# Kernel tuning notes

Hardware: AMD Instinct MI355X
Metric: run time of the kernel (lower is better)

Reference implementation:

```python
import jax, jax.numpy as jnp
import numpy as np

B, H, W = 2, 1024, 1024
NNZ = 100000          # active pixels
C = 16                # max electron count bins (dense dim of sparse logits)
CIN, CH = 128, 128    # in_pixel_features, beta_distn_hidden_dim
THR = 0.95            # count_cdf_threshold
QMAX = NNZ * (C - 1)  # static upper bound on ragged query count


def setup_inputs() -> dict:
    key = jax.random.key(0)
    ks = jax.random.split(key, 4)
    rng = np.random.default_rng(0)
    per = NNZ // B
    idx_list = []
    for b in range(B):
        flat = np.sort(rng.choice(H * W, per, replace=False))  # unique active sites
        idx_list.append(np.stack([np.full(per, b), flat // W, flat % W]))
    occ_indices = jnp.asarray(np.concatenate(idx_list, 1), jnp.int32)  # [3, NNZ]
    occ_values = jax.random.normal(ks[0], (NNZ, C), jnp.float32) * 2.0
    pixel_values = jax.random.normal(ks[1], (NNZ, CIN), jnp.float32)
    w1 = jax.random.normal(ks[2], (3, 3, CIN, CH), jnp.float32) / np.sqrt(9 * CIN)
    b1 = jnp.zeros((CH,), jnp.float32)
    w2 = jax.random.normal(ks[3], (CH, 4), jnp.float32) / np.sqrt(CH)
    b2 = jnp.zeros((4,), jnp.float32)
    return dict(occ_values=occ_values, occ_indices=occ_indices,
                pixel_values=pixel_values, w1=w1, b1=b1, w2=w2, b2=b2)


def reference(occ_values, occ_indices, pixel_values, w1, b1, w2, b2):
    # --- cdf_threshold_min_predicted_electrons ---
    probs = jax.nn.softmax(occ_values, -1)                      # sparse softmax over dense count dim
    cdf = jnp.cumsum(probs, -1)
    over = cdf > THR
    temp = jnp.arange(C, 0, -1) * over
    counts = jnp.argmax(temp, 1)                                # [NNZ] min count over cdf threshold

    # --- repeat_interleave(indices, counts) -> padded ragged queries ---
    cum = jnp.cumsum(counts)
    total = cum[-1]
    q = jnp.arange(QMAX)
    valid = q < total
    src = jnp.minimum(jnp.searchsorted(cum, q, side='right'), NNZ - 1)  # [QMAX]
    query_indices = occ_indices[:, src].T                       # [QMAX, 3] (b, i, j)

    # --- dense hash grid: (b,i,j) -> active-site row ---
    b_, i_, j_ = occ_indices
    flat = (b_ * H + i_) * W + j_
    grid = jnp.full((B * H * W,), -1, jnp.int32).at[flat].set(
        jnp.arange(NNZ, dtype=jnp.int32))

    # --- SubMConv2d(CIN->CH, k=3): output at active sites only ---
    acc = jnp.zeros((NNZ, CH), pixel_values.dtype) + b1
    for di in (-1, 0, 1):
        for dj in (-1, 0, 1):
            ni, nj = i_ + di, j_ + dj
            inb = (ni >= 0) & (ni < H) & (nj >= 0) & (nj < W)
            nflat = (b_ * H + jnp.clip(ni, 0, H - 1)) * W + jnp.clip(nj, 0, W - 1)
            nidx = jnp.where(inb, grid[nflat], -1)
            m = nidx >= 0
            feat = jnp.where(m[:, None], pixel_values[jnp.maximum(nidx, 0)], 0.0)
            acc = acc + feat @ w1[di + 1, dj + 1]
    h = jax.nn.relu(acc)
    logp = h @ w2 + b2                                          # [NNZ, 4] SubMConv2d(CH->4, k=1)

    # --- gather_from_sparse_tensor at query pixels ---
    qflat = (query_indices[:, 0] * H + query_indices[:, 1]) * W + query_indices[:, 2]
    row = jnp.maximum(grid[qflat], 0)
    params = jnp.exp(logp[row])                                 # [QMAX, 4]
    xa, xb, ya, yb = jnp.split(params, 4, -1)

    # --- Beta rsample (reparameterized gamma-based sampler) ---
    k1, k2 = jax.random.split(jax.random.key(42))
    x = jax.random.beta(k1, xa, xb)
    y = jax.random.beta(k2, ya, yb)
    off = jnp.concatenate([x, y], -1) * valid[:, None]          # [QMAX, 2]
    query_indices = jnp.where(valid[:, None], query_indices, 0)
    return query_indices, off
```

## Files before the change

kernel.cpp:

```cpp
#include <hip/hip_runtime.h>
#include <cstdint>

#define NNZ   100000
#define CBINS 16
#define HD    1024
#define WD    1024
#define CIN   128
#define CH    128
#define QMAX  (NNZ * (CBINS - 1))

struct Key { uint32_t a, b; };

__device__ __forceinline__ uint32_t rotl32(uint32_t v, int r) {
  return (v << r) | (v >> (32 - r));
}

__device__ __forceinline__ void tf_block(uint32_t k0, uint32_t k1,
                                         uint32_t x0, uint32_t x1,
                                         uint32_t& o0, uint32_t& o1) {
  uint32_t ks2 = k0 ^ k1 ^ 0x1BD11BDAu;
  x0 += k0; x1 += k1;
#define TF_RND(r) { x0 += x1; x1 = rotl32(x1, r); x1 ^= x0; }
  TF_RND(13) TF_RND(15) TF_RND(26) TF_RND(6)
  x0 += k1;  x1 += ks2 + 1u;
  TF_RND(17) TF_RND(29) TF_RND(16) TF_RND(24)
  x0 += ks2; x1 += k0 + 2u;
  TF_RND(13) TF_RND(15) TF_RND(26) TF_RND(6)
  x0 += k0;  x1 += k1 + 3u;
  TF_RND(17) TF_RND(29) TF_RND(16) TF_RND(24)
  x0 += k1;  x1 += ks2 + 4u;
  TF_RND(13) TF_RND(15) TF_RND(26) TF_RND(6)
  x0 += ks2; x1 += k0 + 5u;
#undef TF_RND
  o0 = x0; o1 = x1;
}

__device__ __forceinline__ Key tf_key(Key k, uint32_t chi, uint32_t clo) {
  Key r; tf_block(k.a, k.b, chi, clo, r.a, r.b); return r;
}

__device__ __forceinline__ uint32_t random_bits32(Key k) {
  uint32_t a, b; tf_block(k.a, k.b, 0u, 0u, a, b); return a ^ b;
}

__device__ __forceinline__ float bits_to_u01(uint32_t bits) {
  uint32_t fb = (bits >> 9) | 0x3F800000u;
  return __uint_as_float(fb) - 1.0f;
}

__device__ float erfinv32(float x) {
#pragma clang fp contract(off)
  float w = -log1pf(-(x * x));
  float p;
  if (w < 5.0f) {
    w = w - 2.5f;
    p = 2.81022636e-08f;
    p = 3.43273939e-07f  + p * w;
    p = -3.5233877e-06f  + p * w;
    p = -4.39150654e-06f + p * w;
    p = 0.00021858087f   + p * w;
    p = -0.00125372503f  + p * w;
    p = -0.00417768164f  + p * w;
    p = 0.246640727f     + p * w;
    p = 1.50140941f      + p * w;
  } else {
    w = sqrtf(w) - 3.0f;
    p = -0.000200214257f;
    p = 0.000100950558f  + p * w;
    p = 0.00134934322f   + p * w;
    p = -0.00367342844f  + p * w;
    p = 0.00573950773f   + p * w;
    p = -0.0076224613f   + p * w;
    p = 0.00943887047f   + p * w;
    p = 1.00167406f      + p * w;
    p = 2.83297682f      + p * w;
  }
  return p * x;
}

__device__ __forceinline__ float uniform01(Key k) {
  return bits_to_u01(random_bits32(k));
}

__device__ __forceinline__ float normal_f32(Key k) {
#pragma clang fp contract(off)
  const float LO = -0x1.fffffep-1f;
  float f = bits_to_u01(random_bits32(k));
  float u = f * 2.0f + LO;
  u = fmaxf(LO, u);
  return 1.4142135623730951f * erfinv32(u);
}

__device__ float loggamma_one(Key key, float alpha_orig) {
#pragma clang fp contract(off)
  bool boost = (alpha_orig >= 1.0f);
  float alpha = boost ? alpha_orig : (alpha_orig + 1.0f);
  const float OT = 0.3333333333333333f;
  float d = alpha - OT;
  float c = OT / sqrtf(d);

  Key knext = tf_key(key, 0u, 0u);
  Key ksub  = tf_key(key, 0u, 1u);
  float u_boost = uniform01(ksub);

  float X = 0.0f, V = 1.0f, U = 2.0f;
  while (true) {
    bool c1 = U >= (1.0f - 0.0331f * (X * X));
    bool c2 = logf(U) >= (X * 0.5f + d * ((1.0f - V) + logf(V)));
    if (!(c1 && c2)) break;
    Key kcur = knext;
    knext    = tf_key(kcur, 0u, 0u);
    Key xk   = tf_key(kcur, 0u, 1u);
    Key Uk   = tf_key(kcur, 0u, 2u);
    float x = 0.0f, v = -1.0f;
    while (v <= 0.0f) {
      Key nxk = tf_key(xk, 0u, 0u);
      Key sk  = tf_key(xk, 0u, 1u);
      xk = nxk;
      x = normal_f32(sk);
      v = 1.0f + x * c;
    }
    X = x * x;
    V = (v * v) * v;
    U = uniform01(Uk);
  }
  float log_samples = logf(d) + logf(V);
  float log_boost = 0.0f;
  if (!boost && u_boost != 0.0f)
    log_boost = logf(u_boost) * (1.0f / alpha_orig);
  return log_samples + log_boost;
}

__device__ float beta_sample(Key ka, Key kb, uint32_t q, float a, float b) {
#pragma clang fp contract(off)
  Key ga = tf_key(ka, 0u, q);
  Key gb = tf_key(kb, 0u, q);
  float la = loggamma_one(ga, a);
  float lb = loggamma_one(gb, b);
  float lm = fmaxf(la, lb);
  float ea = expf(la - lm);
  float eb = expf(lb - lm);
  return ea / (ea + eb);
}


__device__ __forceinline__ void ascan16(const float* a, float* out) {
  float r[8], r2[4], r3[2];
#pragma unroll
  for (int i = 0; i < 8; ++i) r[i] = a[2 * i] + a[2 * i + 1];
#pragma unroll
  for (int i = 0; i < 4; ++i) r2[i] = r[2 * i] + r[2 * i + 1];
  r3[0] = r2[0] + r2[1];
  r3[1] = r2[2] + r2[3];
  float r4 = r3[0] + r3[1];
  float s3[2] = {r3[0], r4};
  float s2[4] = {r2[0], s3[0], s3[0] + r2[2], s3[1]};
  float sr[8] = {r[0],          s2[0],
                 s2[0] + r[2],  s2[1],
                 s2[1] + r[4],  s2[2],
                 s2[2] + r[6],  s2[3]};
  out[0] = a[0];
#pragma unroll
  for (int i = 0; i < 8; ++i) out[2 * i + 1] = sr[i];
#pragma unroll
  for (int i = 0; i < 7; ++i) out[2 * i + 2] = sr[i] + a[2 * i + 2];
}

__global__ __launch_bounds__(256)
void counts_kernel(const float* __restrict__ occ_values,
                   const int* __restrict__ occ_idx,
                   int* __restrict__ counts,
                   int* __restrict__ flatall) {
  int i = blockIdx.x * 256 + threadIdx.x;
  if (i >= NNZ) return;
  const float4* vp = (const float4*)(occ_values + (size_t)i * CBINS);
  float4 q0 = vp[0], q1 = vp[1], q2 = vp[2], q3 = vp[3];
  float v[16] = {q0.x,q0.y,q0.z,q0.w, q1.x,q1.y,q1.z,q1.w,
                 q2.x,q2.y,q2.z,q2.w, q3.x,q3.y,q3.z,q3.w};
  float m = v[0];
#pragma unroll
  for (int k = 1; k < 16; ++k) m = fmaxf(m, v[k]);
  float e[16];
#pragma unroll
  for (int k = 0; k < 16; ++k) e[k] = expf(v[k] - m);
  float s = 0.0f;
#pragma unroll
  for (int k = 0; k < 16; ++k) s += e[k];
  float p[16], cdf[16];
#pragma unroll
  for (int k = 0; k < 16; ++k) p[k] = e[k] / s;
  ascan16(p, cdf);
  int cnt = 0; bool found = false;
#pragma unroll
  for (int k = 0; k < 16; ++k) {
    if (!found && cdf[k] > 0.95f) { found = true; cnt = k; }
  }
  counts[i] = found ? cnt : 0;
  int b_ = occ_idx[i], i_ = occ_idx[NNZ + i], j_ = occ_idx[2 * NNZ + i];
  flatall[i] = (b_ * HD + i_) * WD + j_;
}

#define SCAN_B 1024
__global__ __launch_bounds__(SCAN_B)
void scan_block_kernel(const int* __restrict__ counts, int* __restrict__ cum,
                       int* __restrict__ bsums) {
  __shared__ int sh[SCAN_B];
  int t = threadIdx.x;
  int i = blockIdx.x * SCAN_B + t;
  sh[t] = (i < NNZ) ? counts[i] : 0;
  __syncthreads();
  for (int off = 1; off < SCAN_B; off <<= 1) {
    int add = (t >= off) ? sh[t - off] : 0;
    __syncthreads();
    sh[t] += add;
    __syncthreads();
  }
  if (i < NNZ) cum[i] = sh[t];
  if (t == SCAN_B - 1) bsums[blockIdx.x] = sh[t];
}

__global__ void scan_sums_kernel(int* bsums, int nblocks) {
  __shared__ int sh[128];
  int t = threadIdx.x;
  sh[t] = (t < nblocks) ? bsums[t] : 0;
  __syncthreads();
  for (int off = 1; off < 128; off <<= 1) {
    int add = (t >= off) ? sh[t - off] : 0;
    __syncthreads();
    sh[t] += add;
    __syncthreads();
  }
  if (t < nblocks) bsums[t] = sh[t];
}

__global__ __launch_bounds__(SCAN_B)
void scan_add_kernel(int* cum, const int* __restrict__ bsums) {
  int b = blockIdx.x;
  if (b == 0) return;
  int i = b * SCAN_B + threadIdx.x;
  if (i < NNZ) cum[i] += bsums[b - 1];
}

__device__ __forceinline__ int find_site(const int* __restrict__ flatall, int tval) {
  int lo = 0, hi = NNZ;
  while (lo < hi) {
    int mid = (lo + hi) >> 1;
    if (flatall[mid] < tval) lo = mid + 1; else hi = mid;
  }
  return (lo < NNZ && flatall[lo] == tval) ? lo : -1;
}

__global__ __launch_bounds__(256)
void neighbors_kernel(const int* __restrict__ occ_idx,
                      const int* __restrict__ flatall,
                      int* __restrict__ rlist) {
  int s = blockIdx.x * 256 + threadIdx.x;
  if (s >= NNZ) return;
  int b_ = occ_idx[s], i_ = occ_idx[NNZ + s], j_ = occ_idx[2 * NNZ + s];
  int m = 0;
#pragma unroll
  for (int di = -1; di <= 1; ++di) {
#pragma unroll
    for (int dj = -1; dj <= 1; ++dj) {
      if (di == 0 && dj == 0) continue;
      int ni = i_ + di, nj = j_ + dj, r = -1;
      if ((unsigned)ni < HD && (unsigned)nj < WD)
        r = find_site(flatall, (b_ * HD + ni) * WD + nj);
      rlist[(size_t)s * 8 + m] = r;
      ++m;
    }
  }
}

__global__ __launch_bounds__(256)
void scatter_src_kernel(const int* __restrict__ counts,
                        const int* __restrict__ cum,
                        int* __restrict__ srcmap) {
  int s = blockIdx.x * 256 + threadIdx.x;
  if (s >= NNZ) return;
  int e = cum[s], c = counts[s];
  for (int q = e - c; q < e; ++q) srcmap[q] = s;
}

#define TSITES 64
#define HP     132
__global__ __launch_bounds__(256, 4)
void conv_fused_kernel(const float* __restrict__ pv,
                       const float* __restrict__ w1,
                       const float* __restrict__ b1,
                       const float* __restrict__ w2,
                       const float* __restrict__ b2,
                       const int* __restrict__ rlist,
                       float* __restrict__ logp) {
  __shared__ float smem[TSITES * HP];
  __shared__ int rl[TSITES * 8];
  float* Wsh = smem;
  float* h0  = smem;

  int base = blockIdx.x * TSITES;
  int t = threadIdx.x;

#pragma unroll
  for (int rep = 0; rep < 2; ++rep) {
    int e = t + rep * 256;
    int sc = base + (e >> 3);
    if (sc > NNZ - 1) sc = NNZ - 1;
    rl[e] = rlist[(size_t)sc * 8 + (e & 7)];
  }

  int ts = t >> 5, to = t & 31;
  float acc[8][4];
  {
    float4 bv = *(const float4*)(b1 + to * 4);
#pragma unroll
    for (int s8 = 0; s8 < 8; ++s8) {
      acc[s8][0] = bv.x; acc[s8][1] = bv.y; acc[s8][2] = bv.z; acc[s8][3] = bv.w;
    }
  }

  const float* prow[8];
#pragma unroll
  for (int s8 = 0; s8 < 8; ++s8) {
    int site = base + s8 * 8 + ts;
    if (site > NNZ - 1) site = NNZ - 1;
    prow[s8] = pv + (size_t)site * CIN;
  }

  const float* wc = w1 + 4 * CIN * CH;
  for (int k0 = 0; k0 < CIN; k0 += 32) {
    __syncthreads();
    {
      const float4* srcw = (const float4*)(wc + (size_t)k0 * CH);
      float4* dstw = (float4*)Wsh;
#pragma unroll
      for (int rep = 0; rep < 4; ++rep) dstw[t + rep * 256] = srcw[t + rep * 256];
    }
    __syncthreads();
#pragma unroll
    for (int kk = 0; kk < 32; kk += 4) {
      float4 wq0 = ((const float4*)(Wsh + (kk + 0) * CH))[to];
      float4 wq1 = ((const float4*)(Wsh + (kk + 1) * CH))[to];
      float4 wq2 = ((const float4*)(Wsh + (kk + 2) * CH))[to];
      float4 wq3 = ((const float4*)(Wsh + (kk + 3) * CH))[to];
#pragma unroll
      for (int s8 = 0; s8 < 8; ++s8) {
        float4 a4 = *(const float4*)(prow[s8] + k0 + kk);
        acc[s8][0] += a4.x * wq0.x; acc[s8][1] += a4.x * wq0.y;
        acc[s8][2] += a4.x * wq0.z; acc[s8][3] += a4.x * wq0.w;
        acc[s8][0] += a4.y * wq1.x; acc[s8][1] += a4.y * wq1.y;
        acc[s8][2] += a4.y * wq1.z; acc[s8][3] += a4.y * wq1.w;
        acc[s8][0] += a4.z * wq2.x; acc[s8][1] += a4.z * wq2.y;
        acc[s8][2] += a4.z * wq2.z; acc[s8][3] += a4.z * wq2.w;
        acc[s8][0] += a4.w * wq3.x; acc[s8][1] += a4.w * wq3.y;
        acc[s8][2] += a4.w * wq3.z; acc[s8][3] += a4.w * wq3.w;
      }
    }
  }

  __syncthreads();
#pragma unroll
  for (int s8 = 0; s8 < 8; ++s8) {
    *(float4*)(h0 + (s8 * 8 + ts) * HP + 4 * to) =
        make_float4(acc[s8][0], acc[s8][1], acc[s8][2], acc[s8][3]);
  }
  __syncthreads();

  int w = t >> 6, l = t & 63;
  for (int si = 0; si < 16; ++si) {
    int s = w * 16 + si;
    int site = base + s;
    if (site >= NNZ) break;
    float2 hv = *(const float2*)(h0 + s * HP + 2 * l);
    float ha = hv.x, hb = hv.y;
#pragma unroll
    for (int m = 0; m < 8; ++m) {
      int r = rl[s * 8 + m];
      if (r < 0) continue;
      int tap = (m < 4) ? m : m + 1;
      const float* wt = w1 + (size_t)tap * CIN * CH + 2 * l;
      const float* pr = pv + (size_t)r * CIN;
#pragma unroll 8
      for (int k = 0; k < CIN; k += 4) {
        float4 pq = *(const float4*)(pr + k);
        float2 wv0 = *(const float2*)(wt + (k + 0) * CH);
        float2 wv1 = *(const float2*)(wt + (k + 1) * CH);
        float2 wv2 = *(const float2*)(wt + (k + 2) * CH);
        float2 wv3 = *(const float2*)(wt + (k + 3) * CH);
        ha += pq.x * wv0.x; hb += pq.x * wv0.y;
        ha += pq.y * wv1.x; hb += pq.y * wv1.y;
        ha += pq.z * wv2.x; hb += pq.z * wv2.y;
        ha += pq.w * wv3.x; hb += pq.w * wv3.y;
      }
    }
    *(float2*)(h0 + s * HP + 2 * l) = make_float2(ha, hb);
  }
  __syncthreads();

  {
    int s = t & 63, j = t >> 6;
    int site = base + s;
    if (site < NNZ) {
      const float* hr = h0 + s * HP;
      float sum = 0.0f;
      for (int o = 0; o < CH; o += 2) {
        float2 hv = *(const float2*)(hr + o);
        sum += fmaxf(hv.x, 0.f) * w2[(o + 0) * 4 + j];
        sum += fmaxf(hv.y, 0.f) * w2[(o + 1) * 4 + j];
      }
      logp[(size_t)site * 4 + j] = sum + b2[j];
    }
  }
}

__global__ __launch_bounds__(256)
void query_kernel(const int* __restrict__ occ_idx,
                  const int* __restrict__ cum,
                  const int* __restrict__ srcmap,
                  const float* __restrict__ logp,
                  float* __restrict__ out_idx,
                  float* __restrict__ out_off) {
  int q = blockIdx.x * 256 + threadIdx.x;
  if (q >= QMAX) return;
  int total = cum[NNZ - 1];
  if (q >= total) {
    out_idx[(size_t)q * 3 + 0] = 0.0f;
    out_idx[(size_t)q * 3 + 1] = 0.0f;
    out_idx[(size_t)q * 3 + 2] = 0.0f;
    out_off[(size_t)q * 2 + 0] = 0.0f;
    out_off[(size_t)q * 2 + 1] = 0.0f;
    return;
  }
  int src = srcmap[q];
  out_idx[(size_t)q * 3 + 0] = (float)occ_idx[src];
  out_idx[(size_t)q * 3 + 1] = (float)occ_idx[NNZ + src];
  out_idx[(size_t)q * 3 + 2] = (float)occ_idx[2 * NNZ + src];

  float4 lp = *(const float4*)(logp + (size_t)src * 4);
  float p0 = expf(lp.x), p1 = expf(lp.y), p2 = expf(lp.z), p3 = expf(lp.w);

  Key root{0u, 42u};
  Key k1  = tf_key(root, 0u, 0u);
  Key k2  = tf_key(root, 0u, 1u);
  Key kxa = tf_key(k1, 0u, 0u);
  Key kxb = tf_key(k1, 0u, 1u);
  Key kya = tf_key(k2, 0u, 0u);
  Key kyb = tf_key(k2, 0u, 1u);

  float x = beta_sample(kxa, kxb, (uint32_t)q, p0, p1);
  float y = beta_sample(kya, kyb, (uint32_t)q, p2, p3);
  out_off[(size_t)q * 2 + 0] = x;
  out_off[(size_t)q * 2 + 1] = y;
}

extern "C" void kernel_launch(void* const* d_in, const int* in_sizes, int n_in,
                              void* d_out, int out_size, void* d_ws, size_t ws_size,
                              hipStream_t stream) {
  const float* occ_values = (const float*)d_in[0];
  const int*   occ_idx    = (const int*)d_in[1];
  const float* pv         = (const float*)d_in[2];
  const float* w1         = (const float*)d_in[3];
  const float* b1         = (const float*)d_in[4];
  const float* w2         = (const float*)d_in[5];
  const float* b2         = (const float*)d_in[6];

  char* ws = (char*)d_ws;
  auto alignup = [](size_t x) { return (x + 255) & ~(size_t)255; };
  size_t o = 0;
  int* counts  = (int*)(ws + o); o += alignup((size_t)NNZ * 4);
  int* cum     = (int*)(ws + o); o += alignup((size_t)NNZ * 4);
  int* flatall = (int*)(ws + o); o += alignup((size_t)NNZ * 4);
  int* bsums   = (int*)(ws + o); o += alignup(128 * 4);
  float* logp  = (float*)(ws + o); o += alignup((size_t)NNZ * 4 * sizeof(float));
  int* rlist   = (int*)(ws + o); o += alignup((size_t)NNZ * 8 * 4);
  int* srcmap  = (int*)(ws + o); o += alignup((size_t)QMAX * 4);

  float* out_idx = (float*)d_out;
  float* out_off = out_idx + (size_t)QMAX * 3;

  counts_kernel<<<(NNZ + 255) / 256, 256, 0, stream>>>(occ_values, occ_idx,
                                                       counts, flatall);
  int nsb = (NNZ + SCAN_B - 1) / SCAN_B;
  scan_block_kernel<<<nsb, SCAN_B, 0, stream>>>(counts, cum, bsums);
  scan_sums_kernel<<<1, 128, 0, stream>>>(bsums, nsb);
  scan_add_kernel<<<nsb, SCAN_B, 0, stream>>>(cum, bsums);
  neighbors_kernel<<<(NNZ + 255) / 256, 256, 0, stream>>>(occ_idx, flatall, rlist);
  scatter_src_kernel<<<(NNZ + 255) / 256, 256, 0, stream>>>(counts, cum, srcmap);
  conv_fused_kernel<<<(NNZ + TSITES - 1) / TSITES, 256, 0, stream>>>(
      pv, w1, b1, w2, b2, rlist, logp);
  query_kernel<<<(QMAX + 255) / 256, 256, 0, stream>>>(occ_idx, cum, srcmap,
                                                       logp, out_idx, out_off);
}
```

Measured before the change: 715.2 us.

## Compact active neighbor sites and software-pipeline neighbor-tap loads in conv kernel

Builds a per-block list of sites that have at least one non-center active neighbor, then lets the four waves stride over only those sites instead of a fixed 16 sites each. This balances work across waves and skips empty sites. The inner CIN loop is also rewritten to prefetch the next 8 input and weight values while computing the current ones, which adds register pressure. The order of sites in the list now depends on atomics, but each site's result does not depend on that order.

```diff
diff --git a/kernel.cpp b/kernel.cpp
--- a/kernel.cpp
+++ b/kernel.cpp
@@ -294,12 +294,15 @@
                        float* __restrict__ logp) {
   __shared__ float smem[TSITES * HP];
   __shared__ int rl[TSITES * 8];
+  __shared__ int asl[TSITES];
+  __shared__ int aslN;
   float* Wsh = smem;
   float* h0  = smem;
 
   int base = blockIdx.x * TSITES;
   int t = threadIdx.x;
 
+  if (t == 0) aslN = 0;
 #pragma unroll
   for (int rep = 0; rep < 2; ++rep) {
     int e = t + rep * 256;
@@ -365,11 +368,21 @@
   }
   __syncthreads();
 
+  if (t < TSITES) {
+    bool any = false;
+#pragma unroll
+    for (int m = 0; m < 8; ++m) any |= (rl[t * 8 + m] >= 0);
+    if (any) {
+      int slot = atomicAdd(&aslN, 1);
+      asl[slot] = t;
+    }
+  }
+  __syncthreads();
+
   int w = t >> 6, l = t & 63;
-  for (int si = 0; si < 16; ++si) {
-    int s = w * 16 + si;
-    int site = base + s;
-    if (site >= NNZ) break;
+  int nact = aslN;
+  for (int e = w; e < nact; e += 4) {
+    int s = asl[e];
     float2 hv = *(const float2*)(h0 + s * HP + 2 * l);
     float ha = hv.x, hb = hv.y;
 #pragma unroll
@@ -379,17 +392,44 @@
       int tap = (m < 4) ? m : m + 1;
       const float* wt = w1 + (size_t)tap * CIN * CH + 2 * l;
       const float* pr = pv + (size_t)r * CIN;
-#pragma unroll 8
-      for (int k = 0; k < CIN; k += 4) {
-        float4 pq = *(const float4*)(pr + k);
-        float2 wv0 = *(const float2*)(wt + (k + 0) * CH);
-        float2 wv1 = *(const float2*)(wt + (k + 1) * CH);
-        float2 wv2 = *(const float2*)(wt + (k + 2) * CH);
-        float2 wv3 = *(const float2*)(wt + (k + 3) * CH);
-        ha += pq.x * wv0.x; hb += pq.x * wv0.y;
-        ha += pq.y * wv1.x; hb += pq.y * wv1.y;
-        ha += pq.z * wv2.x; hb += pq.z * wv2.y;
-        ha += pq.w * wv3.x; hb += pq.w * wv3.y;
+      float4 pq0 = *(const float4*)(pr + 0);
+      float4 pq1 = *(const float4*)(pr + 4);
+      float2 wv0 = *(const float2*)(wt + 0 * CH);
+      float2 wv1 = *(const float2*)(wt + 1 * CH);
+      float2 wv2 = *(const float2*)(wt + 2 * CH);
+      float2 wv3 = *(const float2*)(wt + 3 * CH);
+      float2 wv4 = *(const float2*)(wt + 4 * CH);
+      float2 wv5 = *(const float2*)(wt + 5 * CH);
+      float2 wv6 = *(const float2*)(wt + 6 * CH);
+      float2 wv7 = *(const float2*)(wt + 7 * CH);
+#pragma unroll
+      for (int k = 0; k < CIN; k += 8) {
+        float4 nq0 = {}, nq1 = {};
+        float2 nv0 = {}, nv1 = {}, nv2 = {}, nv3 = {};
+        float2 nv4 = {}, nv5 = {}, nv6 = {}, nv7 = {};
+        if (k + 8 < CIN) {
+          nq0 = *(const float4*)(pr + k + 8);
+          nq1 = *(const float4*)(pr + k + 12);
+          nv0 = *(const float2*)(wt + (k + 8) * CH);
+          nv1 = *(const float2*)(wt + (k + 9) * CH);
+          nv2 = *(const float2*)(wt + (k + 10) * CH);
+          nv3 = *(const float2*)(wt + (k + 11) * CH);
+          nv4 = *(const float2*)(wt + (k + 12) * CH);
+          nv5 = *(const float2*)(wt + (k + 13) * CH);
+          nv6 = *(const float2*)(wt + (k + 14) * CH);
+          nv7 = *(const float2*)(wt + (k + 15) * CH);
+        }
+        ha += pq0.x * wv0.x; hb += pq0.x * wv0.y;
+        ha += pq0.y * wv1.x; hb += pq0.y * wv1.y;
+        ha += pq0.z * wv2.x; hb += pq0.z * wv2.y;
+        ha += pq0.w * wv3.x; hb += pq0.w * wv3.y;
+        ha += pq1.x * wv4.x; hb += pq1.x * wv4.y;
+        ha += pq1.y * wv5.x; hb += pq1.y * wv5.y;
+        ha += pq1.z * wv6.x; hb += pq1.z * wv6.y;
+        ha += pq1.w * wv7.x; hb += pq1.w * wv7.y;
+        pq0 = nq0; pq1 = nq1;
+        wv0 = nv0; wv1 = nv1; wv2 = nv2; wv3 = nv3;
+        wv4 = nv4; wv5 = nv5; wv6 = nv6; wv7 = nv7;
       }
     }
     *(float2*)(h0 + s * HP + 2 * l) = make_float2(ha, hb);
```

After: 2.785 ms. 3.89x slower.

## Split fused conv into center GEMM, compacted neighbor correction, and head kernels

Applied to the files above, without the earlier changes.

The fused conv kernel is split into three kernels. One computes the center-tap dense GEMM into a global h buffer. One applies the off-center neighbor taps, but only for sites that have at least one active neighbor; the neighbors kernel compacts those sites with an atomic counter. A separate head kernel then does the ReLU and 1x1 projection. This stops waves from idling over sparse per-site neighbor loops and balances the irregular work across a persistent grid. In exchange it adds a 51 MB round trip of h through global memory and two extra launches.

```diff
diff --git a/kernel.cpp b/kernel.cpp
--- a/kernel.cpp
+++ b/kernel.cpp
@@ -253,11 +253,14 @@
 __global__ __launch_bounds__(256)
 void neighbors_kernel(const int* __restrict__ occ_idx,
                       const int* __restrict__ flatall,
-                      int* __restrict__ rlist) {
+                      int* __restrict__ rlist,
+                      int* __restrict__ asl,
+                      int* __restrict__ nact) {
   int s = blockIdx.x * 256 + threadIdx.x;
   if (s >= NNZ) return;
   int b_ = occ_idx[s], i_ = occ_idx[NNZ + s], j_ = occ_idx[2 * NNZ + s];
   int m = 0;
+  bool any = false;
 #pragma unroll
   for (int di = -1; di <= 1; ++di) {
 #pragma unroll
@@ -267,8 +270,13 @@
       if ((unsigned)ni < HD && (unsigned)nj < WD)
         r = find_site(flatall, (b_ * HD + ni) * WD + nj);
       rlist[(size_t)s * 8 + m] = r;
+      any |= (r >= 0);
       ++m;
     }
+  }
+  if (any) {
+    int slot = atomicAdd(nact, 1);
+    asl[slot] = s;
   }
 }
 
@@ -283,32 +291,16 @@
 }
 
 #define TSITES 64
-#define HP     132
-__global__ __launch_bounds__(256, 4)
-void conv_fused_kernel(const float* __restrict__ pv,
-                       const float* __restrict__ w1,
-                       const float* __restrict__ b1,
-                       const float* __restrict__ w2,
-                       const float* __restrict__ b2,
-                       const int* __restrict__ rlist,
-                       float* __restrict__ logp) {
-  __shared__ float smem[TSITES * HP];
-  __shared__ int rl[TSITES * 8];
-  float* Wsh = smem;
-  float* h0  = smem;
-
+__global__ __launch_bounds__(256)
+void conv_center_kernel(const float* __restrict__ pv,
+                        const float* __restrict__ w1,
+                        const float* __restrict__ b1,
+                        float* __restrict__ h) {
+  __shared__ float Wsh[32 * CH];
   int base = blockIdx.x * TSITES;
   int t = threadIdx.x;
-
-#pragma unroll
-  for (int rep = 0; rep < 2; ++rep) {
-    int e = t + rep * 256;
-    int sc = base + (e >> 3);
-    if (sc > NNZ - 1) sc = NNZ - 1;
-    rl[e] = rlist[(size_t)sc * 8 + (e & 7)];
-  }
-
   int ts = t >> 5, to = t & 31;
+
   float acc[8][4];
   {
     float4 bv = *(const float4*)(b1 + to * 4);
@@ -357,24 +349,35 @@
     }
   }
 
-  __syncthreads();
 #pragma unroll
   for (int s8 = 0; s8 < 8; ++s8) {
-    *(float4*)(h0 + (s8 * 8 + ts) * HP + 4 * to) =
-        make_float4(acc[s8][0], acc[s8][1], acc[s8][2], acc[s8][3]);
-  }
-  __syncthreads();
-
-  int w = t >> 6, l = t & 63;
-  for (int si = 0; si < 16; ++si) {
-    int s = w * 16 + si;
-    int site = base + s;
-    if (site >= NNZ) break;
-    float2 hv = *(const float2*)(h0 + s * HP + 2 * l);
+    int site = base + s8 * 8 + ts;
+    if (site < NNZ)
+      *(float4*)(h + (size_t)site * CH + 4 * to) =
+          make_float4(acc[s8][0], acc[s8][1], acc[s8][2], acc[s8][3]);
+  }
+}
+
+__global__ __launch_bounds__(256)
+void conv_corr_kernel(const float* __restrict__ pv,
+                      const float* __restrict__ w1,
+                      const int* __restrict__ rlist,
+                      const int* __restrict__ asl,
+                      const int* __restrict__ nact,
+                      float* __restrict__ h) {
+  int t = threadIdx.x;
+  int l = t & 63;
+  int wave = (blockIdx.x << 2) + (t >> 6);
+  int nwaves = gridDim.x << 2;
+  int n = *nact;
+  for (int e = wave; e < n; e += nwaves) {
+    int s = asl[e];
+    float* hr = h + (size_t)s * CH;
+    float2 hv = *(const float2*)(hr + 2 * l);
     float ha = hv.x, hb = hv.y;
 #pragma unroll
     for (int m = 0; m < 8; ++m) {
-      int r = rl[s * 8 + m];
+      int r = rlist[(size_t)s * 8 + m];
       if (r < 0) continue;
       int tap = (m < 4) ? m : m + 1;
       const float* wt = w1 + (size_t)tap * CIN * CH + 2 * l;
@@ -392,23 +395,40 @@
         ha += pq.w * wv3.x; hb += pq.w * wv3.y;
       }
     }
-    *(float2*)(h0 + s * HP + 2 * l) = make_float2(ha, hb);
+    *(float2*)(hr + 2 * l) = make_float2(ha, hb);
+  }
+}
+
+#define HP 132
+__global__ __launch_bounds__(256)
+void head_kernel(const float* __restrict__ h,
+                 const float* __restrict__ w2,
+                 const float* __restrict__ b2,
+                 float* __restrict__ logp) {
+  __shared__ float hs[TSITES * HP];
+  int base = blockIdx.x * TSITES;
+  int t = threadIdx.x;
+#pragma unroll
+  for (int rep = 0; rep < 8; ++rep) {
+    int idx = t + rep * 256;
+    int s = idx >> 5, c = idx & 31;
+    int site = base + s;
+    if (site > NNZ - 1) site = NNZ - 1;
+    float4 v = *(const float4*)(h + (size_t)site * CH + 4 * c);
+    *(float4*)(hs + s * HP + 4 * c) = v;
   }
   __syncthreads();
-
-  {
-    int s = t & 63, j = t >> 6;
-    int site = base + s;
-    if (site < NNZ) {
-      const float* hr = h0 + s * HP;
-      float sum = 0.0f;
-      for (int o = 0; o < CH; o += 2) {
-        float2 hv = *(const float2*)(hr + o);
-        sum += fmaxf(hv.x, 0.f) * w2[(o + 0) * 4 + j];
-        sum += fmaxf(hv.y, 0.f) * w2[(o + 1) * 4 + j];
-      }
-      logp[(size_t)site * 4 + j] = sum + b2[j];
-    }
+  int s = t & 63, j = t >> 6;
+  int site = base + s;
+  if (site < NNZ) {
+    const float* hr = hs + s * HP;
+    float sum = 0.0f;
+    for (int o = 0; o < CH; o += 2) {
+      float2 hv = *(const float2*)(hr + o);
+      sum += fmaxf(hv.x, 0.f) * w2[(o + 0) * 4 + j];
+      sum += fmaxf(hv.y, 0.f) * w2[(o + 1) * 4 + j];
+    }
+    logp[(size_t)site * 4 + j] = sum + b2[j];
   }
 }
 
@@ -473,6 +493,9 @@
   float* logp  = (float*)(ws + o); o += alignup((size_t)NNZ * 4 * sizeof(float));
   int* rlist   = (int*)(ws + o); o += alignup((size_t)NNZ * 8 * 4);
   int* srcmap  = (int*)(ws + o); o += alignup((size_t)QMAX * 4);
+  int* asl     = (int*)(ws + o); o += alignup((size_t)NNZ * 4);
+  int* nact    = (int*)(ws + o); o += alignup(256);
+  float* h     = (float*)(ws + o); o += alignup((size_t)NNZ * CH * sizeof(float));
 
   float* out_idx = (float*)d_out;
   float* out_off = out_idx + (size_t)QMAX * 3;
@@ -483,10 +506,14 @@
   scan_block_kernel<<<nsb, SCAN_B, 0, stream>>>(counts, cum, bsums);
   scan_sums_kernel<<<1, 128, 0, stream>>>(bsums, nsb);
   scan_add_kernel<<<nsb, SCAN_B, 0, stream>>>(cum, bsums);
-  neighbors_kernel<<<(NNZ + 255) / 256, 256, 0, stream>>>(occ_idx, flatall, rlist);
+  hipMemsetAsync(nact, 0, 4, stream);
+  neighbors_kernel<<<(NNZ + 255) / 256, 256, 0, stream>>>(occ_idx, flatall,
+                                                          rlist, asl, nact);
   scatter_src_kernel<<<(NNZ + 255) / 256, 256, 0, stream>>>(counts, cum, srcmap);
-  conv_fused_kernel<<<(NNZ + TSITES - 1) / TSITES, 256, 0, stream>>>(
-      pv, w1, b1, w2, b2, rlist, logp);
+  conv_center_kernel<<<(NNZ + TSITES - 1) / TSITES, 256, 0, stream>>>(
+      pv, w1, b1, h);
+  conv_corr_kernel<<<2048, 256, 0, stream>>>(pv, w1, rlist, asl, nact, h);
+  head_kernel<<<(NNZ + TSITES - 1) / TSITES, 256, 0, stream>>>(h, w2, b2, logp);
   query_kernel<<<(QMAX + 255) / 256, 256, 0, stream>>>(occ_idx, cum, srcmap,
                                                        logp, out_idx, out_off);
 }
```

Result: faster. 689.4 us (-3.6%).
